# Performance work log

Hardware: AMD Instinct MI355X
Metric: run time of the kernel (lower is better)

## Reference

```python
import jax, jax.numpy as jnp
import numpy as np

B, N = 2, 250000
C = 64            # feat_channels
VS = (0.1, 0.1, 8.0)
PCR = (-51.2, -51.2, -5.0, 51.2, 51.2, 3.0)
NX = NY = 1024
EPS = 1e-5        # BatchNorm eps
SUB = 128         # cluster points into 128x128 cells -> <=16384 pillars < max_pillars


def setup_inputs() -> dict:
    key = jax.random.key(0)
    ks = jax.random.split(key, 16)
    # clustered pillar coords so unique pillar count stays below max_pillars
    px = jax.random.randint(ks[0], (B, N), 0, SUB)
    py = jax.random.randint(ks[1], (B, N), 0, SUB)
    u = jax.random.uniform(ks[2], (B, N, 2))
    x = PCR[0] + (px.astype(jnp.float32) + u[..., 0]) * VS[0]
    y = PCR[1] + (py.astype(jnp.float32) + u[..., 1]) * VS[1]
    z = jax.random.uniform(ks[3], (B, N), minval=-5.0, maxval=3.0)
    inten = jax.random.uniform(ks[4], (B, N))
    ring = jax.random.uniform(ks[5], (B, N))
    points = jnp.stack([x, y, z, inten, ring], axis=-1).astype(jnp.float32)
    points_mask = jax.random.uniform(ks[6], (B, N)) < 0.9
    # PFN params: Linear(10->64,no bias)+BN+ReLU, Linear(64->64,no bias)+BN+ReLU (BN in eval mode)
    W1 = jax.random.normal(ks[7], (10, C), jnp.float32) * 0.3
    g1 = jax.random.uniform(ks[8], (C,), minval=0.5, maxval=1.5)
    b1 = jax.random.normal(ks[9], (C,)) * 0.1
    m1 = jax.random.normal(ks[10], (C,)) * 0.1
    v1 = jax.random.uniform(ks[11], (C,), minval=0.5, maxval=1.5)
    W2 = jax.random.normal(ks[12], (C, C), jnp.float32) * 0.1
    g2 = jax.random.uniform(ks[13], (C,), minval=0.5, maxval=1.5)
    b2 = jax.random.normal(ks[14], (C,)) * 0.1
    m2 = jax.random.normal(ks[15], (C,)) * 0.1
    v2 = jnp.ones((C,), jnp.float32)
    return dict(points=points, points_mask=points_mask, W1=W1, g1=g1, b1=b1, m1=m1, v1=v1,
                W2=W2, g2=g2, b2=b2, m2=m2, v2=v2)


def reference(points, points_mask, W1, g1, b1, m1, v1, W2, g2, b2, m2, v2):
    mask = points_mask.astype(points.dtype)                       # (B,N)
    x, y, z = points[..., 0], points[..., 1], points[..., 2]
    px = jnp.clip(jnp.floor((x - PCR[0]) / VS[0]).astype(jnp.int32), 0, NX - 1)
    py = jnp.clip(jnp.floor((y - PCR[1]) / VS[1]).astype(jnp.int32), 0, NY - 1)
    idx = py * NX + px                                            # (B,N) flat pillar index
    # mean z over valid points per batch element
    z_mean = (z * mask).sum(-1) / jnp.maximum(mask.sum(-1), 1.0)  # (B,)
    pxf, pyf = px.astype(points.dtype), py.astype(points.dtype)
    x_c = x - (pxf * VS[0] + PCR[0] + VS[0] / 2)
    y_c = y - (pyf * VS[1] + PCR[1] + VS[1] / 2)
    z_c = z - z_mean[:, None]
    x_p = x - (pxf * VS[0] + PCR[0])
    y_p = y - (pyf * VS[1] + PCR[1])
    aug = jnp.concatenate([points, jnp.stack([x_c, y_c, z_c, x_p, y_p], axis=-1)], axis=-1)  # (B,N,10)
    # PFN (BatchNorm in eval mode; pointwise, so safe to apply to all points then mask)
    h = jnp.einsum('bnf,fc->bnc', aug, W1)
    h = jax.nn.relu((h - m1) * (g1 / jnp.sqrt(v1 + EPS)) + b1)
    h = jnp.einsum('bnc,cd->bnd', h, W2)
    h = jax.nn.relu((h - m2) * (g2 / jnp.sqrt(v2 + EPS)) + b2)     # (B,N,C), >=0
    h = h * mask[..., None]                                        # invalid points -> 0 contribution
    # scatter-max into BEV grid; empty cells stay 0 (matches torch: only occupied cells written,
    # and post-ReLU features are >=0 so max(0, feats) == max(feats))
    def scat(idx_b, h_b):
        bev = jnp.zeros((NY * NX, C), h_b.dtype).at[idx_b].max(h_b)
        return bev.T.reshape(C, NY, NX)
    return jax.vmap(scat)(idx, h)                                  # (B,C,NY,NX)
```

## Files before the change

### kernel.cpp

```cpp
#include <hip/hip_runtime.h>

typedef float f32x4 __attribute__((ext_vector_type(4)));
typedef int   i32x4 __attribute__((ext_vector_type(4)));

namespace {
constexpr int   B_    = 2;
constexpr int   N_    = 250000;
constexpr int   C_    = 64;
constexpr int   NX_   = 1024;
constexpr int   NY_   = 1024;
constexpr int   CELLS = NX_ * NY_;
constexpr int   TOT   = B_ * CELLS;
constexpr float VS0   = 0.1f, VS1 = 0.1f;
constexpr float PC0   = -51.2f, PC1 = -51.2f;
constexpr float EPS_  = 1e-5f;

constexpr int   PBLK  = (N_ + 255) / 256;
constexpr int   GRID  = 1024;
constexpr int   NSTRIPE = (B_ * C_ * CELLS) / 2048;

constexpr int WS_W1T  = 0;
constexpr int WS_B1   = 640;
constexpr int WS_W2T  = 704;
constexpr int WS_B2   = 4800;
constexpr int WS_PZ   = 4864;
constexpr int WS_PM   = WS_PZ + 2048;
constexpr int WS_CNT  = WS_PM + 2048;
constexpr int WS_HEAD = 16384;
constexpr int WS_NEXT = WS_HEAD + TOT;
constexpr int WS_LIST = WS_NEXT + B_ * N_;
constexpr int WS_BMP  = WS_LIST + B_ * N_;
constexpr int WS_END  = WS_BMP + TOT / 32;
constexpr size_t NEED_BYTES = (size_t)WS_END * 4;
}

__global__ __launch_bounds__(256) void init_prep(const float* __restrict__ W1, const float* __restrict__ g1,
                                                 const float* __restrict__ b1, const float* __restrict__ m1,
                                                 const float* __restrict__ v1, const float* __restrict__ W2,
                                                 const float* __restrict__ g2, const float* __restrict__ b2,
                                                 const float* __restrict__ m2, const float* __restrict__ v2,
                                                 float* __restrict__ wsf, int* __restrict__ wsi) {
    const int tid    = blockIdx.x * 256 + threadIdx.x;
    const int stride = gridDim.x * 256;
    i32x4* head4 = (i32x4*)(wsi + WS_HEAD);
    i32x4* bmp4  = (i32x4*)(wsi + WS_BMP);
    const i32x4 mone = {-1, -1, -1, -1};
    const i32x4 zero = {0, 0, 0, 0};
    for (int i = tid; i < TOT / 4; i += stride) __builtin_nontemporal_store(mone, head4 + i);
    for (int i = tid; i < TOT / 32 / 4; i += stride) __builtin_nontemporal_store(zero, bmp4 + i);
    if (tid < 1024) ((i32x4*)(wsi + WS_PZ))[tid] = zero;
    if (tid == 0) wsi[WS_CNT] = 0;
    if (blockIdx.x == 0 && threadIdx.x < C_) {
        const int c = threadIdx.x;
        float s1 = g1[c] / sqrtf(v1[c] + EPS_);
        for (int f = 0; f < 10; ++f) wsf[WS_W1T + c * 10 + f] = W1[f * C_ + c] * s1;
        wsf[WS_B1 + c] = b1[c] - m1[c] * s1;
        float s2 = g2[c] / sqrtf(v2[c] + EPS_);
        for (int k = 0; k < C_; ++k) wsf[WS_W2T + c * C_ + k] = W2[k * C_ + c] * s2;
        wsf[WS_B2 + c] = b2[c] - m2[c] * s2;
    }
}

__device__ __forceinline__ int cell_of(float x, float y) {
    int px = (int)floorf((x - PC0) / VS0);
    int py = (int)floorf((y - PC1) / VS1);
    px = px < 0 ? 0 : (px > NX_ - 1 ? NX_ - 1 : px);
    py = py < 0 ? 0 : (py > NY_ - 1 ? NY_ - 1 : py);
    return py * NX_ + px;
}

__global__ __launch_bounds__(256) void pass1(const float* __restrict__ pts,
                                             const int* __restrict__ mask,
                                             float* __restrict__ wsf, int* __restrict__ wsi) {
    const int b = blockIdx.y, t = threadIdx.x;
    const int n = blockIdx.x * 256 + t;
    float sz = 0.f, sm = 0.f;
    if (n < N_ && mask[b * N_ + n]) {
        const size_t pb = ((size_t)b * N_ + n) * 5;
        const float x = pts[pb], y = pts[pb + 1], z = pts[pb + 2];
        const int idx = b * CELLS + cell_of(x, y);
        const int old = atomicExch(&wsi[WS_HEAD + idx], n);
        wsi[WS_NEXT + b * N_ + n] = old;
        if (old == -1) {
            const int li = atomicAdd(&wsi[WS_CNT], 1);
            wsi[WS_LIST + li] = idx;
            atomicOr(&wsi[WS_BMP + (idx >> 5)], 1 << (idx & 31));
        }
        sz = z; sm = 1.f;
    }
    __shared__ float lz[256], lm[256];
    lz[t] = sz; lm[t] = sm;
    __syncthreads();
    for (int s = 128; s > 0; s >>= 1) {
        if (t < s) { lz[t] += lz[t + s]; lm[t] += lm[t + s]; }
        __syncthreads();
    }
    if (t == 0) { wsf[WS_PZ + b * 1024 + blockIdx.x] = lz[0]; wsf[WS_PM + b * 1024 + blockIdx.x] = lm[0]; }
}

__global__ __launch_bounds__(256) void fat(const float* __restrict__ pts,
                                           const float* __restrict__ wsf,
                                           const int* __restrict__ wsi,
                                           float* __restrict__ out) {
    __shared__ float red[16];
    const int t    = threadIdx.x;
    const int wid  = t >> 6;
    const int lane = t & 63;
    const int c    = lane;

    float sz0 = 0.f, sm0 = 0.f, sz1 = 0.f, sm1 = 0.f;
#pragma unroll
    for (int k = 0; k < 4; ++k) {
        const int i = t + k * 256;
        sz0 += wsf[WS_PZ + i];        sm0 += wsf[WS_PM + i];
        sz1 += wsf[WS_PZ + 1024 + i]; sm1 += wsf[WS_PM + 1024 + i];
    }
#pragma unroll
    for (int m = 32; m >= 1; m >>= 1) {
        sz0 += __shfl_xor(sz0, m, 64); sm0 += __shfl_xor(sm0, m, 64);
        sz1 += __shfl_xor(sz1, m, 64); sm1 += __shfl_xor(sm1, m, 64);
    }
    if (lane == 0) {
        red[wid * 4 + 0] = sz0; red[wid * 4 + 1] = sm0;
        red[wid * 4 + 2] = sz1; red[wid * 4 + 3] = sm1;
    }
    __syncthreads();
    const float zm0 = (red[0] + red[4] + red[8] + red[12]) /
                      fmaxf(red[1] + red[5] + red[9] + red[13], 1.f);
    const float zm1 = (red[2] + red[6] + red[10] + red[14]) /
                      fmaxf(red[3] + red[7] + red[11] + red[15], 1.f);

    float w1c[10];
#pragma unroll
    for (int f = 0; f < 10; ++f) w1c[f] = wsf[WS_W1T + c * 10 + f];
    const float b1c = wsf[WS_B1 + c];
    float w2c[C_];
#pragma unroll
    for (int k = 0; k < C_; ++k) w2c[k] = wsf[WS_W2T + c * C_ + k];
    const float b2c = wsf[WS_B2 + c];

    const int W  = blockIdx.x * 4 + wid;
    const int NW = GRID * 4;
    const int cnt = wsi[WS_CNT];
    for (int e = W; e < cnt; e += NW) {
        const int idx  = wsi[WS_LIST + e];
        const int b    = idx >> 20;
        const int cell = idx & (CELLS - 1);
        const float pxf = (float)(cell & (NX_ - 1));
        const float pyf = (float)(cell >> 10);
        const float zmean = b ? zm1 : zm0;
        float hmax = 0.f;
        int n = wsi[WS_HEAD + idx];
        while (n != -1) {
            const int nx = wsi[WS_NEXT + b * N_ + n];
            const size_t pb = ((size_t)b * N_ + n) * 5;
            const float x = pts[pb], y = pts[pb + 1], z = pts[pb + 2];
            const float it = pts[pb + 3], rg = pts[pb + 4];
            float a = b1c;
            a = fmaf(x,  w1c[0], a);
            a = fmaf(y,  w1c[1], a);
            a = fmaf(z,  w1c[2], a);
            a = fmaf(it, w1c[3], a);
            a = fmaf(rg, w1c[4], a);
            a = fmaf(x - (pxf * VS0 + PC0 + VS0 * 0.5f), w1c[5], a);
            a = fmaf(y - (pyf * VS1 + PC1 + VS1 * 0.5f), w1c[6], a);
            a = fmaf(z - zmean,                          w1c[7], a);
            a = fmaf(x - (pxf * VS0 + PC0),              w1c[8], a);
            a = fmaf(y - (pyf * VS1 + PC1),              w1c[9], a);
            const int h1i = __float_as_int(fmaxf(a, 0.f));
            float ac0 = 0.f, ac1 = 0.f, ac2 = 0.f, ac3 = 0.f;
#pragma unroll
            for (int k = 0; k < 16; ++k) {
                ac0 = fmaf(__int_as_float(__builtin_amdgcn_readlane(h1i, 4 * k + 0)), w2c[4 * k + 0], ac0);
                ac1 = fmaf(__int_as_float(__builtin_amdgcn_readlane(h1i, 4 * k + 1)), w2c[4 * k + 1], ac1);
                ac2 = fmaf(__int_as_float(__builtin_amdgcn_readlane(h1i, 4 * k + 2)), w2c[4 * k + 2], ac2);
                ac3 = fmaf(__int_as_float(__builtin_amdgcn_readlane(h1i, 4 * k + 3)), w2c[4 * k + 3], ac3);
            }
            hmax = fmaxf(hmax, b2c + ((ac0 + ac1) + (ac2 + ac3)));
            n = nx;
        }
        out[(((size_t)b * C_ + c) << 20) + cell] = hmax;
    }

    f32x4* out4 = (f32x4*)out;
    const f32x4 z4 = {0.f, 0.f, 0.f, 0.f};
    for (int s = W; s < NSTRIPE; s += NW) {
        const int p  = s >> 9;
        const int q  = s & 511;
        const int bb = p >> 6;
        const int Wd = wsi[WS_BMP + bb * (CELLS / 32) + q * 64 + lane];
        const int ib = (p << 18) + (q << 9);
        if (__ballot(Wd != 0) == 0ULL) {
#pragma unroll
            for (int k = 0; k < 8; ++k)
                __builtin_nontemporal_store(z4, out4 + (ib + k * 64 + lane));
        } else {
#pragma unroll
            for (int k = 0; k < 8; ++k) {
                const unsigned w   = (unsigned)__shfl(Wd, k * 8 + (lane >> 3), 64);
                const unsigned nib = (w >> ((lane & 7) * 4)) & 0xFu;
                const int i = ib + k * 64 + lane;
                if (nib == 0u) {
                    __builtin_nontemporal_store(z4, out4 + i);
                } else {
#pragma unroll
                    for (int jj = 0; jj < 4; ++jj)
                        if (!((nib >> jj) & 1u)) out[(size_t)i * 4 + jj] = 0.f;
                }
            }
        }
    }
}

__global__ void prep_weights_fb(const float* __restrict__ W1, const float* __restrict__ g1,
                                const float* __restrict__ b1, const float* __restrict__ m1,
                                const float* __restrict__ v1, const float* __restrict__ W2,
                                const float* __restrict__ g2, const float* __restrict__ b2,
                                const float* __restrict__ m2, const float* __restrict__ v2,
                                float* __restrict__ ws) {
    int c = threadIdx.x;
    if (c >= C_) return;
    float s1 = g1[c] / sqrtf(v1[c] + EPS_);
    for (int f = 0; f < 10; ++f) ws[WS_W1T + c * 10 + f] = W1[f * C_ + c] * s1;
    ws[WS_B1 + c] = b1[c] - m1[c] * s1;
    float s2 = g2[c] / sqrtf(v2[c] + EPS_);
    for (int k = 0; k < C_; ++k) ws[WS_W2T + c * C_ + k] = W2[k * C_ + c] * s2;
    ws[WS_B2 + c] = b2[c] - m2[c] * s2;
}

__global__ void zmean_fb1(const float* __restrict__ pts, const int* __restrict__ mask,
                          float* __restrict__ ws) {
    const int b = blockIdx.y, t = threadIdx.x;
    const int n = blockIdx.x * 256 + t;
    float sz = 0.f, sm = 0.f;
    if (n < N_ && mask[b * N_ + n]) {
        sz = pts[((size_t)b * N_ + n) * 5 + 2];
        sm = 1.f;
    }
    __shared__ float lz[256], lm[256];
    lz[t] = sz; lm[t] = sm;
    __syncthreads();
    for (int s = 128; s > 0; s >>= 1) {
        if (t < s) { lz[t] += lz[t + s]; lm[t] += lm[t + s]; }
        __syncthreads();
    }
    if (t == 0) { ws[WS_PZ + b * 1024 + blockIdx.x] = lz[0]; ws[WS_PM + b * 1024 + blockIdx.x] = lm[0]; }
}

__global__ void zmean_fb2(float* __restrict__ ws) {
    const int b = blockIdx.x, t = threadIdx.x;
    __shared__ float lz[256], lm[256];
    float sz = 0.f, sm = 0.f;
    for (int k = t; k < 1024; k += 256) {
        sz += (k < PBLK) ? ws[WS_PZ + b * 1024 + k] : 0.f;
        sm += (k < PBLK) ? ws[WS_PM + b * 1024 + k] : 0.f;
    }
    lz[t] = sz; lm[t] = sm;
    __syncthreads();
    for (int s = 128; s > 0; s >>= 1) {
        if (t < s) { lz[t] += lz[t + s]; lm[t] += lm[t + s]; }
        __syncthreads();
    }
    if (t == 0) ws[WS_CNT + 2 + b] = lz[0] / fmaxf(lm[0], 1.f);
}

__global__ __launch_bounds__(256) void pfn_scatter_fb(const float* __restrict__ pts,
                                                      const int* __restrict__ mask,
                                                      const float* __restrict__ ws,
                                                      float* __restrict__ out) {
    const int b = blockIdx.y;
    const int n = blockIdx.x * 256 + threadIdx.x;
    if (n >= N_) return;
    if (!mask[b * N_ + n]) return;
    const float zmean = ws[WS_CNT + 2 + b];
    const size_t pbase = ((size_t)b * N_ + n) * 5;
    const float x = pts[pbase], y = pts[pbase + 1], z = pts[pbase + 2];
    const float it = pts[pbase + 3], rg = pts[pbase + 4];
    const int cell = cell_of(x, y);
    const float pxf = (float)(cell & (NX_ - 1)), pyf = (float)(cell >> 10);
    float aug[10];
    aug[0] = x; aug[1] = y; aug[2] = z; aug[3] = it; aug[4] = rg;
    aug[5] = x - (pxf * VS0 + PC0 + VS0 * 0.5f);
    aug[6] = y - (pyf * VS1 + PC1 + VS1 * 0.5f);
    aug[7] = z - zmean;
    aug[8] = x - (pxf * VS0 + PC0);
    aug[9] = y - (pyf * VS1 + PC1);
    float h1[C_];
#pragma unroll
    for (int c = 0; c < C_; ++c) {
        float acc = ws[WS_B1 + c];
#pragma unroll
        for (int f = 0; f < 10; ++f) acc = fmaf(aug[f], ws[WS_W1T + c * 10 + f], acc);
        h1[c] = fmaxf(acc, 0.f);
    }
    unsigned int* ob = (unsigned int*)out + (size_t)b * C_ * CELLS + cell;
#pragma unroll 4
    for (int c = 0; c < C_; ++c) {
        float acc = ws[WS_B2 + c];
#pragma unroll
        for (int k = 0; k < C_; ++k) acc = fmaf(h1[k], ws[WS_W2T + c * C_ + k], acc);
        if (acc > 0.f) atomicMax(ob + (size_t)c * CELLS, __float_as_uint(acc));
    }
}

extern "C" void kernel_launch(void* const* d_in, const int* in_sizes, int n_in,
                              void* d_out, int out_size, void* d_ws, size_t ws_size,
                              hipStream_t stream) {
    const float* pts  = (const float*)d_in[0];
    const int*   mask = (const int*)d_in[1];
    const float* W1 = (const float*)d_in[2];
    const float* g1 = (const float*)d_in[3];
    const float* b1 = (const float*)d_in[4];
    const float* m1 = (const float*)d_in[5];
    const float* v1 = (const float*)d_in[6];
    const float* W2 = (const float*)d_in[7];
    const float* g2 = (const float*)d_in[8];
    const float* b2 = (const float*)d_in[9];
    const float* m2 = (const float*)d_in[10];
    const float* v2 = (const float*)d_in[11];
    float* wsf = (float*)d_ws;
    int*   wsi = (int*)d_ws;
    float* out = (float*)d_out;

    if (ws_size >= NEED_BYTES) {
        init_prep<<<512, 256, 0, stream>>>(W1, g1, b1, m1, v1, W2, g2, b2, m2, v2, wsf, wsi);
        pass1<<<dim3(PBLK, B_), 256, 0, stream>>>(pts, mask, wsf, wsi);
        fat<<<GRID, 256, 0, stream>>>(pts, wsf, wsi, out);
    } else {
        hipMemsetAsync(d_out, 0, (size_t)out_size * sizeof(float), stream);
        hipMemsetAsync((char*)d_ws + (size_t)WS_PZ * 4, 0, 4096 * 4, stream);
        prep_weights_fb<<<1, 256, 0, stream>>>(W1, g1, b1, m1, v1, W2, g2, b2, m2, v2, wsf);
        zmean_fb1<<<dim3(PBLK, B_), 256, 0, stream>>>(pts, mask, wsf);
        zmean_fb2<<<B_, 256, 0, stream>>>(wsf);
        pfn_scatter_fb<<<dim3((N_ + 255) / 256, B_), 256, 0, stream>>>(pts, mask, wsf, out);
    }
}
```

Before: 239.1 us.

## Interleave two pillar linked-list walks per wave and alternate compute/zero role order

Each wave now walks two pillars' point linked lists at once, issuing both next-pointer loads before the per-point MLP work. This hides the dependent pointer-chasing latency. Odd waves also run the zero-fill stripe pass before the compute pass, so memory-heavy stores overlap with compute-heavy MLP work across the GPU. The paired walk adds divergence when the two lists differ in length and raises register pressure.

```diff
diff --git a/kernel.cpp b/kernel.cpp
--- a/kernel.cpp
+++ b/kernel.cpp
@@ -141,75 +141,96 @@
 
     const int W  = blockIdx.x * 4 + wid;
     const int NW = GRID * 4;
-    const int cnt = wsi[WS_CNT];
-    for (int e = W; e < cnt; e += NW) {
-        const int idx  = wsi[WS_LIST + e];
-        const int b    = idx >> 20;
-        const int cell = idx & (CELLS - 1);
-        const float pxf = (float)(cell & (NX_ - 1));
-        const float pyf = (float)(cell >> 10);
-        const float zmean = b ? zm1 : zm0;
-        float hmax = 0.f;
-        int n = wsi[WS_HEAD + idx];
-        while (n != -1) {
-            const int nx = wsi[WS_NEXT + b * N_ + n];
-            const size_t pb = ((size_t)b * N_ + n) * 5;
-            const float x = pts[pb], y = pts[pb + 1], z = pts[pb + 2];
-            const float it = pts[pb + 3], rg = pts[pb + 4];
-            float a = b1c;
-            a = fmaf(x,  w1c[0], a);
-            a = fmaf(y,  w1c[1], a);
-            a = fmaf(z,  w1c[2], a);
-            a = fmaf(it, w1c[3], a);
-            a = fmaf(rg, w1c[4], a);
-            a = fmaf(x - (pxf * VS0 + PC0 + VS0 * 0.5f), w1c[5], a);
-            a = fmaf(y - (pyf * VS1 + PC1 + VS1 * 0.5f), w1c[6], a);
-            a = fmaf(z - zmean,                          w1c[7], a);
-            a = fmaf(x - (pxf * VS0 + PC0),              w1c[8], a);
-            a = fmaf(y - (pyf * VS1 + PC1),              w1c[9], a);
-            const int h1i = __float_as_int(fmaxf(a, 0.f));
-            float ac0 = 0.f, ac1 = 0.f, ac2 = 0.f, ac3 = 0.f;
-#pragma unroll
-            for (int k = 0; k < 16; ++k) {
-                ac0 = fmaf(__int_as_float(__builtin_amdgcn_readlane(h1i, 4 * k + 0)), w2c[4 * k + 0], ac0);
-                ac1 = fmaf(__int_as_float(__builtin_amdgcn_readlane(h1i, 4 * k + 1)), w2c[4 * k + 1], ac1);
-                ac2 = fmaf(__int_as_float(__builtin_amdgcn_readlane(h1i, 4 * k + 2)), w2c[4 * k + 2], ac2);
-                ac3 = fmaf(__int_as_float(__builtin_amdgcn_readlane(h1i, 4 * k + 3)), w2c[4 * k + 3], ac3);
+
+    auto visit = [&](int n, int b, float pxf, float pyf, float zmean, float& hmax) {
+        const size_t pb = ((size_t)b * N_ + n) * 5;
+        const float x = pts[pb], y = pts[pb + 1], z = pts[pb + 2];
+        const float it = pts[pb + 3], rg = pts[pb + 4];
+        float a = b1c;
+        a = fmaf(x,  w1c[0], a);
+        a = fmaf(y,  w1c[1], a);
+        a = fmaf(z,  w1c[2], a);
+        a = fmaf(it, w1c[3], a);
+        a = fmaf(rg, w1c[4], a);
+        a = fmaf(x - (pxf * VS0 + PC0 + VS0 * 0.5f), w1c[5], a);
+        a = fmaf(y - (pyf * VS1 + PC1 + VS1 * 0.5f), w1c[6], a);
+        a = fmaf(z - zmean,                          w1c[7], a);
+        a = fmaf(x - (pxf * VS0 + PC0),              w1c[8], a);
+        a = fmaf(y - (pyf * VS1 + PC1),              w1c[9], a);
+        const int h1i = __float_as_int(fmaxf(a, 0.f));
+        float ac0 = 0.f, ac1 = 0.f, ac2 = 0.f, ac3 = 0.f;
+#pragma unroll
+        for (int k = 0; k < 16; ++k) {
+            ac0 = fmaf(__int_as_float(__builtin_amdgcn_readlane(h1i, 4 * k + 0)), w2c[4 * k + 0], ac0);
+            ac1 = fmaf(__int_as_float(__builtin_amdgcn_readlane(h1i, 4 * k + 1)), w2c[4 * k + 1], ac1);
+            ac2 = fmaf(__int_as_float(__builtin_amdgcn_readlane(h1i, 4 * k + 2)), w2c[4 * k + 2], ac2);
+            ac3 = fmaf(__int_as_float(__builtin_amdgcn_readlane(h1i, 4 * k + 3)), w2c[4 * k + 3], ac3);
+        }
+        hmax = fmaxf(hmax, b2c + ((ac0 + ac1) + (ac2 + ac3)));
+    };
+
+    auto compute_role = [&]() {
+        const int cnt = wsi[WS_CNT];
+        for (int e = W; e < cnt; e += 2 * NW) {
+            const int eB    = e + NW;
+            const bool hasB = eB < cnt;
+            const int idxA  = wsi[WS_LIST + e];
+            const int idxB  = hasB ? wsi[WS_LIST + eB] : idxA;
+            const int bA    = idxA >> 20,          bB   = idxB >> 20;
+            const int cellA = idxA & (CELLS - 1),  cellB = idxB & (CELLS - 1);
+            const float pxfA = (float)(cellA & (NX_ - 1)), pxfB = (float)(cellB & (NX_ - 1));
+            const float pyfA = (float)(cellA >> 10),       pyfB = (float)(cellB >> 10);
+            const float zmA  = bA ? zm1 : zm0,             zmB  = bB ? zm1 : zm0;
+            float hmaxA = 0.f, hmaxB = 0.f;
+            int nA = wsi[WS_HEAD + idxA];
+            int nB = hasB ? wsi[WS_HEAD + idxB] : -1;
+            while (nA != -1 || nB != -1) {
+                int nxA = -1, nxB = -1;
+                if (nA != -1) nxA = wsi[WS_NEXT + bA * N_ + nA];
+                if (nB != -1) nxB = wsi[WS_NEXT + bB * N_ + nB];
+                if (nA != -1) visit(nA, bA, pxfA, pyfA, zmA, hmaxA);
+                if (nB != -1) visit(nB, bB, pxfB, pyfB, zmB, hmaxB);
+                nA = (nA != -1) ? nxA : -1;
+                nB = (nB != -1) ? nxB : -1;
             }
-            hmax = fmaxf(hmax, b2c + ((ac0 + ac1) + (ac2 + ac3)));
-            n = nx;
+            out[(((size_t)bA * C_ + c) << 20) + cellA] = hmaxA;
+            if (hasB) out[(((size_t)bB * C_ + c) << 20) + cellB] = hmaxB;
         }
-        out[(((size_t)b * C_ + c) << 20) + cell] = hmax;
-    }
-
-    f32x4* out4 = (f32x4*)out;
-    const f32x4 z4 = {0.f, 0.f, 0.f, 0.f};
-    for (int s = W; s < NSTRIPE; s += NW) {
-        const int p  = s >> 9;
-        const int q  = s & 511;
-        const int bb = p >> 6;
-        const int Wd = wsi[WS_BMP + bb * (CELLS / 32) + q * 64 + lane];
-        const int ib = (p << 18) + (q << 9);
-        if (__ballot(Wd != 0) == 0ULL) {
-#pragma unroll
-            for (int k = 0; k < 8; ++k)
-                __builtin_nontemporal_store(z4, out4 + (ib + k * 64 + lane));
-        } else {
-#pragma unroll
-            for (int k = 0; k < 8; ++k) {
-                const unsigned w   = (unsigned)__shfl(Wd, k * 8 + (lane >> 3), 64);
-                const unsigned nib = (w >> ((lane & 7) * 4)) & 0xFu;
-                const int i = ib + k * 64 + lane;
-                if (nib == 0u) {
-                    __builtin_nontemporal_store(z4, out4 + i);
-                } else {
-#pragma unroll
-                    for (int jj = 0; jj < 4; ++jj)
-                        if (!((nib >> jj) & 1u)) out[(size_t)i * 4 + jj] = 0.f;
+    };
+
+    auto zero_role = [&]() {
+        f32x4* out4 = (f32x4*)out;
+        const f32x4 z4 = {0.f, 0.f, 0.f, 0.f};
+        for (int s = W; s < NSTRIPE; s += NW) {
+            const int p  = s >> 9;
+            const int q  = s & 511;
+            const int bb = p >> 6;
+            const int Wd = wsi[WS_BMP + bb * (CELLS / 32) + q * 64 + lane];
+            const int ib = (p << 18) + (q << 9);
+            if (__ballot(Wd != 0) == 0ULL) {
+#pragma unroll
+                for (int k = 0; k < 8; ++k)
+                    __builtin_nontemporal_store(z4, out4 + (ib + k * 64 + lane));
+            } else {
+#pragma unroll
+                for (int k = 0; k < 8; ++k) {
+                    const unsigned w   = (unsigned)__shfl(Wd, k * 8 + (lane >> 3), 64);
+                    const unsigned nib = (w >> ((lane & 7) * 4)) & 0xFu;
+                    const int i = ib + k * 64 + lane;
+                    if (nib == 0u) {
+                        __builtin_nontemporal_store(z4, out4 + i);
+                    } else {
+#pragma unroll
+                        for (int jj = 0; jj < 4; ++jj)
+                            if (!((nib >> jj) & 1u)) out[(size_t)i * 4 + jj] = 0.f;
+                    }
                 }
             }
         }
-    }
+    };
+
+    if (W & 1) { zero_role(); compute_role(); }
+    else       { compute_role(); zero_role(); }
 }
 
 __global__ void prep_weights_fb(const float* __restrict__ W1, const float* __restrict__ g1,
```

Result: slower. 253.8 us (+6.2%).

## Split per-pillar linked lists into four interleaved chains for memory-level parallelism

Applied to the files above, without the earlier changes.

Each pillar now keeps four head pointers, chosen by the low bits of the point index, so the fat kernel can walk four independent chains at once. Four next-pointer loads are in flight per step instead of one serialized load per point. The pillar is now marked first-seen by testing the old bitmap bit from atomicOr rather than the exchanged head value. The cost is a head array four times larger, which the init kernel must fill with -1, plus extra branching in the walk loop.

```diff
diff --git a/kernel.cpp b/kernel.cpp
--- a/kernel.cpp
+++ b/kernel.cpp
@@ -18,6 +18,7 @@
 constexpr int   PBLK  = (N_ + 255) / 256;
 constexpr int   GRID  = 1024;
 constexpr int   NSTRIPE = (B_ * C_ * CELLS) / 2048;
+constexpr int   NSUB  = 4;
 
 constexpr int WS_W1T  = 0;
 constexpr int WS_B1   = 640;
@@ -27,7 +28,7 @@
 constexpr int WS_PM   = WS_PZ + 2048;
 constexpr int WS_CNT  = WS_PM + 2048;
 constexpr int WS_HEAD = 16384;
-constexpr int WS_NEXT = WS_HEAD + TOT;
+constexpr int WS_NEXT = WS_HEAD + TOT * NSUB;
 constexpr int WS_LIST = WS_NEXT + B_ * N_;
 constexpr int WS_BMP  = WS_LIST + B_ * N_;
 constexpr int WS_END  = WS_BMP + TOT / 32;
@@ -46,7 +47,7 @@
     i32x4* bmp4  = (i32x4*)(wsi + WS_BMP);
     const i32x4 mone = {-1, -1, -1, -1};
     const i32x4 zero = {0, 0, 0, 0};
-    for (int i = tid; i < TOT / 4; i += stride) __builtin_nontemporal_store(mone, head4 + i);
+    for (int i = tid; i < TOT * NSUB / 4; i += stride) __builtin_nontemporal_store(mone, head4 + i);
     for (int i = tid; i < TOT / 32 / 4; i += stride) __builtin_nontemporal_store(zero, bmp4 + i);
     if (tid < 1024) ((i32x4*)(wsi + WS_PZ))[tid] = zero;
     if (tid == 0) wsi[WS_CNT] = 0;
@@ -79,12 +80,14 @@
         const size_t pb = ((size_t)b * N_ + n) * 5;
         const float x = pts[pb], y = pts[pb + 1], z = pts[pb + 2];
         const int idx = b * CELLS + cell_of(x, y);
-        const int old = atomicExch(&wsi[WS_HEAD + idx], n);
+        const int j   = n & (NSUB - 1);
+        const int old = atomicExch(&wsi[WS_HEAD + idx * NSUB + j], n);
         wsi[WS_NEXT + b * N_ + n] = old;
-        if (old == -1) {
+        const int bit = 1 << (idx & 31);
+        const int ob  = atomicOr(&wsi[WS_BMP + (idx >> 5)], bit);
+        if (!(ob & bit)) {
             const int li = atomicAdd(&wsi[WS_CNT], 1);
             wsi[WS_LIST + li] = idx;
-            atomicOr(&wsi[WS_BMP + (idx >> 5)], 1 << (idx & 31));
         }
         sz = z; sm = 1.f;
     }
@@ -141,71 +144,92 @@
 
     const int W  = blockIdx.x * 4 + wid;
     const int NW = GRID * 4;
-    const int cnt = wsi[WS_CNT];
-    for (int e = W; e < cnt; e += NW) {
-        const int idx  = wsi[WS_LIST + e];
-        const int b    = idx >> 20;
-        const int cell = idx & (CELLS - 1);
-        const float pxf = (float)(cell & (NX_ - 1));
-        const float pyf = (float)(cell >> 10);
-        const float zmean = b ? zm1 : zm0;
-        float hmax = 0.f;
-        int n = wsi[WS_HEAD + idx];
-        while (n != -1) {
-            const int nx = wsi[WS_NEXT + b * N_ + n];
-            const size_t pb = ((size_t)b * N_ + n) * 5;
-            const float x = pts[pb], y = pts[pb + 1], z = pts[pb + 2];
-            const float it = pts[pb + 3], rg = pts[pb + 4];
-            float a = b1c;
-            a = fmaf(x,  w1c[0], a);
-            a = fmaf(y,  w1c[1], a);
-            a = fmaf(z,  w1c[2], a);
-            a = fmaf(it, w1c[3], a);
-            a = fmaf(rg, w1c[4], a);
-            a = fmaf(x - (pxf * VS0 + PC0 + VS0 * 0.5f), w1c[5], a);
-            a = fmaf(y - (pyf * VS1 + PC1 + VS1 * 0.5f), w1c[6], a);
-            a = fmaf(z - zmean,                          w1c[7], a);
-            a = fmaf(x - (pxf * VS0 + PC0),              w1c[8], a);
-            a = fmaf(y - (pyf * VS1 + PC1),              w1c[9], a);
-            const int h1i = __float_as_int(fmaxf(a, 0.f));
-            float ac0 = 0.f, ac1 = 0.f, ac2 = 0.f, ac3 = 0.f;
-#pragma unroll
-            for (int k = 0; k < 16; ++k) {
-                ac0 = fmaf(__int_as_float(__builtin_amdgcn_readlane(h1i, 4 * k + 0)), w2c[4 * k + 0], ac0);
-                ac1 = fmaf(__int_as_float(__builtin_amdgcn_readlane(h1i, 4 * k + 1)), w2c[4 * k + 1], ac1);
-                ac2 = fmaf(__int_as_float(__builtin_amdgcn_readlane(h1i, 4 * k + 2)), w2c[4 * k + 2], ac2);
-                ac3 = fmaf(__int_as_float(__builtin_amdgcn_readlane(h1i, 4 * k + 3)), w2c[4 * k + 3], ac3);
+
+    {
+        const int cnt = wsi[WS_CNT];
+        for (int e = W; e < cnt; e += NW) {
+            const int idx  = wsi[WS_LIST + e];
+            const int b    = idx >> 20;
+            const int cell = idx & (CELLS - 1);
+            const float pxf = (float)(cell & (NX_ - 1));
+            const float pyf = (float)(cell >> 10);
+            const float zmean = b ? zm1 : zm0;
+            const int nbase = b * N_;
+            float hmax = 0.f;
+            int n0 = wsi[WS_HEAD + idx * NSUB + 0];
+            int n1 = wsi[WS_HEAD + idx * NSUB + 1];
+            int n2 = wsi[WS_HEAD + idx * NSUB + 2];
+            int n3 = wsi[WS_HEAD + idx * NSUB + 3];
+
+            auto visit = [&](int n) {
+                const size_t pb = ((size_t)nbase + n) * 5;
+                const float x = pts[pb], y = pts[pb + 1], z = pts[pb + 2];
+                const float it = pts[pb + 3], rg = pts[pb + 4];
+                float a = b1c;
+                a = fmaf(x,  w1c[0], a);
+                a = fmaf(y,  w1c[1], a);
+                a = fmaf(z,  w1c[2], a);
+                a = fmaf(it, w1c[3], a);
+                a = fmaf(rg, w1c[4], a);
+                a = fmaf(x - (pxf * VS0 + PC0 + VS0 * 0.5f), w1c[5], a);
+                a = fmaf(y - (pyf * VS1 + PC1 + VS1 * 0.5f), w1c[6], a);
+                a = fmaf(z - zmean,                          w1c[7], a);
+                a = fmaf(x - (pxf * VS0 + PC0),              w1c[8], a);
+                a = fmaf(y - (pyf * VS1 + PC1),              w1c[9], a);
+                const int h1i = __float_as_int(fmaxf(a, 0.f));
+                float ac0 = 0.f, ac1 = 0.f, ac2 = 0.f, ac3 = 0.f;
+#pragma unroll
+                for (int k = 0; k < 16; ++k) {
+                    ac0 = fmaf(__int_as_float(__builtin_amdgcn_readlane(h1i, 4 * k + 0)), w2c[4 * k + 0], ac0);
+                    ac1 = fmaf(__int_as_float(__builtin_amdgcn_readlane(h1i, 4 * k + 1)), w2c[4 * k + 1], ac1);
+                    ac2 = fmaf(__int_as_float(__builtin_amdgcn_readlane(h1i, 4 * k + 2)), w2c[4 * k + 2], ac2);
+                    ac3 = fmaf(__int_as_float(__builtin_amdgcn_readlane(h1i, 4 * k + 3)), w2c[4 * k + 3], ac3);
+                }
+                hmax = fmaxf(hmax, b2c + ((ac0 + ac1) + (ac2 + ac3)));
+            };
+
+            while ((n0 != -1) | (n1 != -1) | (n2 != -1) | (n3 != -1)) {
+                int nx0 = -1, nx1 = -1, nx2 = -1, nx3 = -1;
+                if (n0 != -1) nx0 = wsi[WS_NEXT + nbase + n0];
+                if (n1 != -1) nx1 = wsi[WS_NEXT + nbase + n1];
+                if (n2 != -1) nx2 = wsi[WS_NEXT + nbase + n2];
+                if (n3 != -1) nx3 = wsi[WS_NEXT + nbase + n3];
+                if (n0 != -1) visit(n0);
+                if (n1 != -1) visit(n1);
+                if (n2 != -1) visit(n2);
+                if (n3 != -1) visit(n3);
+                n0 = nx0; n1 = nx1; n2 = nx2; n3 = nx3;
             }
-            hmax = fmaxf(hmax, b2c + ((ac0 + ac1) + (ac2 + ac3)));
-            n = nx;
+            out[(((size_t)b * C_ + c) << 20) + cell] = hmax;
         }
-        out[(((size_t)b * C_ + c) << 20) + cell] = hmax;
-    }
-
-    f32x4* out4 = (f32x4*)out;
-    const f32x4 z4 = {0.f, 0.f, 0.f, 0.f};
-    for (int s = W; s < NSTRIPE; s += NW) {
-        const int p  = s >> 9;
-        const int q  = s & 511;
-        const int bb = p >> 6;
-        const int Wd = wsi[WS_BMP + bb * (CELLS / 32) + q * 64 + lane];
-        const int ib = (p << 18) + (q << 9);
-        if (__ballot(Wd != 0) == 0ULL) {
-#pragma unroll
-            for (int k = 0; k < 8; ++k)
-                __builtin_nontemporal_store(z4, out4 + (ib + k * 64 + lane));
-        } else {
-#pragma unroll
-            for (int k = 0; k < 8; ++k) {
-                const unsigned w   = (unsigned)__shfl(Wd, k * 8 + (lane >> 3), 64);
-                const unsigned nib = (w >> ((lane & 7) * 4)) & 0xFu;
-                const int i = ib + k * 64 + lane;
-                if (nib == 0u) {
-                    __builtin_nontemporal_store(z4, out4 + i);
-                } else {
-#pragma unroll
-                    for (int jj = 0; jj < 4; ++jj)
-                        if (!((nib >> jj) & 1u)) out[(size_t)i * 4 + jj] = 0.f;
+    }
+
+    {
+        f32x4* out4 = (f32x4*)out;
+        const f32x4 z4 = {0.f, 0.f, 0.f, 0.f};
+        for (int s = W; s < NSTRIPE; s += NW) {
+            const int p  = s >> 9;
+            const int q  = s & 511;
+            const int bb = p >> 6;
+            const int Wd = wsi[WS_BMP + bb * (CELLS / 32) + q * 64 + lane];
+            const int ib = (p << 18) + (q << 9);
+            if (__ballot(Wd != 0) == 0ULL) {
+#pragma unroll
+                for (int k = 0; k < 8; ++k)
+                    __builtin_nontemporal_store(z4, out4 + (ib + k * 64 + lane));
+            } else {
+#pragma unroll
+                for (int k = 0; k < 8; ++k) {
+                    const unsigned w   = (unsigned)__shfl(Wd, k * 8 + (lane >> 3), 64);
+                    const unsigned nib = (w >> ((lane & 7) * 4)) & 0xFu;
+                    const int i = ib + k * 64 + lane;
+                    if (nib == 0u) {
+                        __builtin_nontemporal_store(z4, out4 + i);
+                    } else {
+#pragma unroll
+                        for (int jj = 0; jj < 4; ++jj)
+                            if (!((nib >> jj) & 1u)) out[(size_t)i * 4 + jj] = 0.f;
+                    }
                 }
             }
         }
```

After: 262.8 us. 9.9% more time.
